# Kernel tuning notes

Measured on AMD Instinct MI355X. Metric: run time of the kernel, lower is better.

## Reference

```python
import jax, jax.numpy as jnp
import numpy as np

N_NODES = 100000
N_EDGES = 3200000
NODE_DIM = 32
EDGE_DIM = 16
LN_EPS = 1e-5


def setup_inputs() -> dict:
    key = jax.random.key(0)
    ks = jax.random.split(key, 12)
    zdim = 2 * NODE_DIM + EDGE_DIM  # 80
    s_lin = 1.0 / np.sqrt(zdim)
    s_out = 1.0 / np.sqrt(NODE_DIM)
    return {
        "x": jax.random.normal(ks[0], (N_NODES, NODE_DIM), jnp.float32),
        "edge_index": jax.random.randint(ks[1], (2, N_EDGES), 0, N_NODES, jnp.int32),
        "edge_attr": jax.random.normal(ks[2], (N_EDGES, EDGE_DIM), jnp.float32),
        "edge_weight": jax.random.uniform(ks[3], (N_EDGES,), jnp.float32),
        "lin_f_w": jax.random.uniform(ks[4], (zdim, NODE_DIM), jnp.float32, -s_lin, s_lin),
        "lin_f_b": jax.random.uniform(ks[5], (NODE_DIM,), jnp.float32, -s_lin, s_lin),
        "lin_s_w": jax.random.uniform(ks[6], (zdim, NODE_DIM), jnp.float32, -s_lin, s_lin),
        "lin_s_b": jax.random.uniform(ks[7], (NODE_DIM,), jnp.float32, -s_lin, s_lin),
        "ln_g": jnp.ones((NODE_DIM,), jnp.float32),
        "ln_b": jnp.zeros((NODE_DIM,), jnp.float32),
        "lin_w": jax.random.uniform(ks[8], (NODE_DIM, NODE_DIM), jnp.float32, -s_out, s_out),
        "lin_b": jax.random.uniform(ks[9], (NODE_DIM,), jnp.float32, -s_out, s_out),
    }


def reference(x, edge_index, edge_attr, edge_weight,
              lin_f_w, lin_f_b, lin_s_w, lin_s_b,
              ln_g, ln_b, lin_w, lin_b):
    src, dst = edge_index[0], edge_index[1]  # PyG: x_j = x[src], x_i = x[dst]
    # Gather + concat -> z [E, 2*node_dim + edge_dim]
    z = jnp.concatenate([x[dst], x[src], edge_attr], axis=-1)
    # Dual-linear gate: sigmoid(lin_f(z)) * softplus(lin_s(z)), scaled by edge_weight
    gate = jax.nn.sigmoid(z @ lin_f_w + lin_f_b)
    val = jax.nn.softplus(z @ lin_s_w + lin_s_b)
    msg = edge_weight[:, None] * gate * val  # [E, node_dim]
    # Scatter-add to target nodes
    agg = jax.ops.segment_sum(msg, dst, num_segments=x.shape[0])
    h = agg + x  # conv residual
    # LayerNorm
    mu = jnp.mean(h, axis=-1, keepdims=True)
    var = jnp.var(h, axis=-1, keepdims=True)
    h = (h - mu) * jax.lax.rsqrt(var + LN_EPS) * ln_g + ln_b
    # Linear + residual + ELU
    h = h @ lin_w + lin_b + x
    out = jax.nn.elu(h)
    return (out, edge_index, edge_attr, edge_weight)
```

## Files before the change

### kernel.cpp

```cpp
#include <hip/hip_runtime.h>
#include <hip/hip_fp16.h>
#include <math.h>

#define NODE_DIM 32
#define EDGE_DIM 16
#define WPC 64
#define MAXBLK 2500

typedef __attribute__((ext_vector_type(8))) short bf16x8;
typedef __attribute__((ext_vector_type(4))) short short4v;
typedef __attribute__((ext_vector_type(4))) float f32x4;

__device__ __forceinline__ short f2bf(float f) {
    union { float f; unsigned u; } v; v.f = f;
    unsigned r = v.u + 0x7FFFu + ((v.u >> 16) & 1u);
    return (short)(r >> 16);
}

__device__ __forceinline__ float fast_sigmoid(float v) {
    return __builtin_amdgcn_rcpf(1.0f + __expf(-v));
}
__device__ __forceinline__ float fast_softplus(float v) {
    float t = __expf(-fabsf(v));
    return fmaxf(v, 0.0f) + __logf(1.0f + t);
}

__global__ __launch_bounds__(256) void xconv_kernel(
    const float* __restrict__ x, short* __restrict__ xb, int ngroups)
{
    const int i = blockIdx.x * 256 + threadIdx.x;
    if (i >= ngroups) return;
    const float4* p = (const float4*)x + 2 * (size_t)i;
    float4 u0 = p[0], u1 = p[1];
    bf16x8 o;
    o[0]=f2bf(u0.x); o[1]=f2bf(u0.y); o[2]=f2bf(u0.z); o[3]=f2bf(u0.w);
    o[4]=f2bf(u1.x); o[5]=f2bf(u1.y); o[6]=f2bf(u1.z); o[7]=f2bf(u1.w);
    ((bf16x8*)xb)[i] = o;
}

__global__ __launch_bounds__(256, 4) void edge_kernel(
    const short* __restrict__ xb,
    const int*   __restrict__ ei,
    const float* __restrict__ ea,
    const float* __restrict__ ew,
    const float* __restrict__ Wf,
    const float* __restrict__ bfb,
    const float* __restrict__ Ws,
    const float* __restrict__ bsb,
    __half2* __restrict__ agg2,
    float* __restrict__ out_ei,
    float* __restrict__ out_ea,
    float* __restrict__ out_ew,
    int E)
{
    __shared__ short sea[4][WPC * EDGE_DIM];

    const int tid  = threadIdx.x;
    const int lane = tid & 63;
    const int wave = tid >> 6;
    const int kg   = lane >> 4;
    const int c16  = lane & 15;

    bf16x8 Bf[3][4];
    float biasv[4];
    #pragma unroll
    for (int ct = 0; ct < 4; ++ct) {
        const float* Wsrc = (ct < 2) ? Wf  : Ws;
        const float* bsrc = (ct < 2) ? bfb : bsb;
        const int ccc = 2 * c16 + (ct & 1);
        biasv[ct] = bsrc[ccc];
        #pragma unroll
        for (int m = 0; m < 3; ++m) {
            bf16x8 frag;
            #pragma unroll
            for (int j = 0; j < 8; ++j) {
                const int k = 32 * m + 8 * kg + j;
                const float wv = (k < 80) ? Wsrc[k * NODE_DIM + ccc] : 0.0f;
                frag[j] = f2bf(wv);
            }
            Bf[m][ct] = frag;
        }
    }

    const int wid    = blockIdx.x * 4 + wave;
    const int nwaves = gridDim.x * 4;

    for (int base = wid * WPC; base < E; base += nwaves * WPC) {
        const int e0 = base + lane;
        int srcv = 0, dstv = -1; float wv = 0.0f;
        if (e0 < E) {
            srcv = ei[e0];
            dstv = ei[E + e0];
            wv   = ew[e0];
            out_ei[e0]     = (float)srcv;
            out_ei[E + e0] = (float)dstv;
            out_ew[e0]     = wv;
        }
        {
            const float4* s4 = (const float4*)ea;
            float4*       d4 = (float4*)out_ea;
            const int fmax = E * 4;
            const int fb   = base * 4;
            #pragma unroll
            for (int t = 0; t < 4; ++t) {
                const int idx = fb + t * 64 + lane;
                if (idx < fmax) {
                    float4 v = s4[idx];
                    d4[idx] = v;
                    short4v sv = { f2bf(v.x), f2bf(v.y), f2bf(v.z), f2bf(v.w) };
                    *(short4v*)&sea[wave][(t * 64 + lane) * 4] = sv;
                }
            }
        }

        #pragma unroll 2
        for (int g = 0; g < 4; ++g) {
            const int sA   = g * 16 + c16;
            const int dstn = max(__shfl(dstv, sA), 0);
            const int srcn = max(__shfl(srcv, sA), 0);

            bf16x8 a0 = *(const bf16x8*)(xb + (size_t)dstn * NODE_DIM + 8 * kg);
            bf16x8 a1 = *(const bf16x8*)(xb + (size_t)srcn * NODE_DIM + 8 * kg);
            bf16x8 a2 = {0,0,0,0,0,0,0,0};
            if (kg < 2) {
                a2 = *(const bf16x8*)&sea[wave][sA * EDGE_DIM + 8 * kg];
            }

            f32x4 acc0 = {biasv[0], biasv[0], biasv[0], biasv[0]};
            f32x4 acc1 = {biasv[1], biasv[1], biasv[1], biasv[1]};
            f32x4 acc2 = {biasv[2], biasv[2], biasv[2], biasv[2]};
            f32x4 acc3 = {biasv[3], biasv[3], biasv[3], biasv[3]};

            acc0 = __builtin_amdgcn_mfma_f32_16x16x32_bf16(a0, Bf[0][0], acc0, 0, 0, 0);
            acc1 = __builtin_amdgcn_mfma_f32_16x16x32_bf16(a0, Bf[0][1], acc1, 0, 0, 0);
            acc2 = __builtin_amdgcn_mfma_f32_16x16x32_bf16(a0, Bf[0][2], acc2, 0, 0, 0);
            acc3 = __builtin_amdgcn_mfma_f32_16x16x32_bf16(a0, Bf[0][3], acc3, 0, 0, 0);
            acc0 = __builtin_amdgcn_mfma_f32_16x16x32_bf16(a1, Bf[1][0], acc0, 0, 0, 0);
            acc1 = __builtin_amdgcn_mfma_f32_16x16x32_bf16(a1, Bf[1][1], acc1, 0, 0, 0);
            acc2 = __builtin_amdgcn_mfma_f32_16x16x32_bf16(a1, Bf[1][2], acc2, 0, 0, 0);
            acc3 = __builtin_amdgcn_mfma_f32_16x16x32_bf16(a1, Bf[1][3], acc3, 0, 0, 0);
            acc0 = __builtin_amdgcn_mfma_f32_16x16x32_bf16(a2, Bf[2][0], acc0, 0, 0, 0);
            acc1 = __builtin_amdgcn_mfma_f32_16x16x32_bf16(a2, Bf[2][1], acc1, 0, 0, 0);
            acc2 = __builtin_amdgcn_mfma_f32_16x16x32_bf16(a2, Bf[2][2], acc2, 0, 0, 0);
            acc3 = __builtin_amdgcn_mfma_f32_16x16x32_bf16(a2, Bf[2][3], acc3, 0, 0, 0);

            const int rb = g * 16 + (kg << 2);
            #pragma unroll
            for (int r = 0; r < 4; ++r) {
                const int slot = rb + r;
                const int d    = __shfl(dstv, slot);
                const float w  = __shfl(wv,   slot);
                const float me = w * fast_sigmoid(acc0[r]) * fast_softplus(acc2[r]);
                const float mo = w * fast_sigmoid(acc1[r]) * fast_softplus(acc3[r]);
                if (d >= 0) {
                    __half2 hv = __floats2half2_rn(me, mo);
                    unsafeAtomicAdd(&agg2[(size_t)d * 16 + c16], hv);
                }
            }
        }
    }
}

__global__ __launch_bounds__(256) void node_kernel(
    const float* __restrict__ x,
    const __half2* __restrict__ agg2,
    const float* __restrict__ ln_g,
    const float* __restrict__ ln_b,
    const float* __restrict__ W,
    const float* __restrict__ b,
    float* __restrict__ out,
    int N)
{
    const int n = blockIdx.x * blockDim.x + threadIdx.x;
    if (n >= N) return;

    float xr[NODE_DIM], h[NODE_DIM];
    const float4*  xp = (const float4*)(x + (size_t)n * NODE_DIM);
    const __half2* ah = agg2 + (size_t)n * 16;

    float s = 0.0f, ss = 0.0f;
    #pragma unroll
    for (int i = 0; i < 8; ++i) {
        float4 xv = xp[i];
        float2 f0 = __half22float2(ah[2 * i]);
        float2 f1 = __half22float2(ah[2 * i + 1]);
        float hv0 = xv.x + f0.x, hv1 = xv.y + f0.y, hv2 = xv.z + f1.x, hv3 = xv.w + f1.y;
        xr[4*i+0] = xv.x; xr[4*i+1] = xv.y; xr[4*i+2] = xv.z; xr[4*i+3] = xv.w;
        h[4*i+0] = hv0; h[4*i+1] = hv1; h[4*i+2] = hv2; h[4*i+3] = hv3;
        s  += hv0 + hv1 + hv2 + hv3;
        ss += hv0*hv0 + hv1*hv1 + hv2*hv2 + hv3*hv3;
    }

    const float mu  = s * (1.0f / NODE_DIM);
    float var = ss * (1.0f / NODE_DIM) - mu * mu;
    var = fmaxf(var, 0.0f);
    const float rstd = __builtin_amdgcn_rsqf(var + 1e-5f);

    float acc[NODE_DIM];
    #pragma unroll
    for (int j = 0; j < NODE_DIM; ++j) acc[j] = b[j] + xr[j];

    #pragma unroll
    for (int k = 0; k < NODE_DIM; ++k) {
        float hn = (h[k] - mu) * rstd * ln_g[k] + ln_b[k];
        #pragma unroll
        for (int j = 0; j < NODE_DIM; ++j) {
            acc[j] = fmaf(hn, W[k * NODE_DIM + j], acc[j]);
        }
    }

    float4* op = (float4*)(out + (size_t)n * NODE_DIM);
    #pragma unroll
    for (int i = 0; i < 8; ++i) {
        float4 o;
        float a0 = acc[4*i+0], a1 = acc[4*i+1], a2 = acc[4*i+2], a3 = acc[4*i+3];
        o.x = (a0 > 0.0f) ? a0 : (__expf(a0) - 1.0f);
        o.y = (a1 > 0.0f) ? a1 : (__expf(a1) - 1.0f);
        o.z = (a2 > 0.0f) ? a2 : (__expf(a2) - 1.0f);
        o.w = (a3 > 0.0f) ? a3 : (__expf(a3) - 1.0f);
        op[i] = o;
    }
}

extern "C" void kernel_launch(void* const* d_in, const int* in_sizes, int n_in,
                              void* d_out, int out_size, void* d_ws, size_t ws_size,
                              hipStream_t stream)
{
    const float* x   = (const float*)d_in[0];
    const int*   ei  = (const int*)  d_in[1];
    const float* ea  = (const float*)d_in[2];
    const float* ew  = (const float*)d_in[3];
    const float* Wf  = (const float*)d_in[4];
    const float* bf  = (const float*)d_in[5];
    const float* Ws  = (const float*)d_in[6];
    const float* bs  = (const float*)d_in[7];
    const float* lg  = (const float*)d_in[8];
    const float* lb  = (const float*)d_in[9];
    const float* W   = (const float*)d_in[10];
    const float* b   = (const float*)d_in[11];

    const int E = in_sizes[3];
    const int N = in_sizes[0] / NODE_DIM;

    float* out    = (float*)d_out;
    float* out_x  = out;
    float* out_ei = out + (size_t)N * NODE_DIM;
    float* out_ea = out + (size_t)N * NODE_DIM + 2 * (size_t)E;
    float* out_ew = out_ea + (size_t)E * EDGE_DIM;

    __half2* agg2 = (__half2*)d_ws;
    short*   xbuf = (short*)((char*)d_ws + (size_t)N * 16 * sizeof(__half2));

    hipMemsetAsync(agg2, 0, (size_t)N * 16 * sizeof(__half2), stream);

    const int ngroups = N * NODE_DIM / 8;
    xconv_kernel<<<dim3((ngroups + 255) / 256), dim3(256), 0, stream>>>(x, xbuf, ngroups);

    int nblk = (E + 4 * WPC - 1) / (4 * WPC);
    if (nblk > MAXBLK) nblk = MAXBLK;
    edge_kernel<<<dim3(nblk), dim3(256), 0, stream>>>(
        xbuf, ei, ea, ew, Wf, bf, Ws, bs, agg2, out_ei, out_ea, out_ew, E);

    dim3 nb(256), ng((N + 255) / 256);
    node_kernel<<<ng, nb, 0, stream>>>(x, agg2, lg, lb, W, b, out_x, N);
}
```

Before: 281.9 us.

## Sort edges by destination via counting sort and combine same-node atomics

Adds histogram, two-level scan and scatter kernels that build a permutation grouping edges by destination node. The edge kernel then processes edges in that order and accumulates runs of consecutive edges with the same destination in registers before issuing one half2 atomic, cutting atomic traffic. In exchange it adds several extra kernel launches, a contended atomic histogram and scatter over all edges, a single-thread block-sum scan, and non-coalesced permuted reads of edge_attr and edge_weight.

Result: slower. 865.4 us (+207.0%).

```diff
diff --git a/kernel.cpp b/kernel.cpp
--- a/kernel.cpp
+++ b/kernel.cpp
@@ -6,6 +6,7 @@
 #define EDGE_DIM 16
 #define WPC 64
 #define MAXBLK 2500
+#define SCAN_BS 1024
 
 typedef __attribute__((ext_vector_type(8))) short bf16x8;
 typedef __attribute__((ext_vector_type(4))) short short4v;
@@ -36,6 +37,65 @@
     o[0]=f2bf(u0.x); o[1]=f2bf(u0.y); o[2]=f2bf(u0.z); o[3]=f2bf(u0.w);
     o[4]=f2bf(u1.x); o[5]=f2bf(u1.y); o[6]=f2bf(u1.z); o[7]=f2bf(u1.w);
     ((bf16x8*)xb)[i] = o;
+}
+
+__global__ __launch_bounds__(256) void hist_kernel(
+    const int* __restrict__ ei, int* __restrict__ cnt, int E)
+{
+    const int t = blockIdx.x * 256 + threadIdx.x;
+    if (t < E) atomicAdd(&cnt[ei[E + t]], 1);
+}
+
+__global__ __launch_bounds__(SCAN_BS) void bsum_kernel(
+    const int* __restrict__ cnt, int* __restrict__ bsum, int N)
+{
+    __shared__ int red[SCAN_BS];
+    const int t = blockIdx.x * SCAN_BS + threadIdx.x;
+    red[threadIdx.x] = (t < N) ? cnt[t] : 0;
+    __syncthreads();
+    for (int s = SCAN_BS / 2; s > 0; s >>= 1) {
+        if (threadIdx.x < s) red[threadIdx.x] += red[threadIdx.x + s];
+        __syncthreads();
+    }
+    if (threadIdx.x == 0) bsum[blockIdx.x] = red[0];
+}
+
+__global__ void scanb_kernel(int* __restrict__ bsum, int nb)
+{
+    if (blockIdx.x == 0 && threadIdx.x == 0) {
+        int acc = 0;
+        for (int i = 0; i < nb; ++i) { int v = bsum[i]; bsum[i] = acc; acc += v; }
+    }
+}
+
+__global__ __launch_bounds__(SCAN_BS) void woff_kernel(
+    const int* __restrict__ cnt, const int* __restrict__ bsum,
+    int* __restrict__ woff, int N)
+{
+    __shared__ int sc[SCAN_BS];
+    const int t = blockIdx.x * SCAN_BS + threadIdx.x;
+    const int v = (t < N) ? cnt[t] : 0;
+    sc[threadIdx.x] = v;
+    __syncthreads();
+    for (int s = 1; s < SCAN_BS; s <<= 1) {
+        int add = (threadIdx.x >= s) ? sc[threadIdx.x - s] : 0;
+        __syncthreads();
+        sc[threadIdx.x] += add;
+        __syncthreads();
+    }
+    if (t < N) woff[t] = bsum[blockIdx.x] + sc[threadIdx.x] - v;
+}
+
+__global__ __launch_bounds__(256) void scatter_kernel(
+    const int* __restrict__ ei, int* __restrict__ woff,
+    int* __restrict__ perm, int E)
+{
+    const int t = blockIdx.x * 256 + threadIdx.x;
+    if (t < E) {
+        const int d = ei[E + t];
+        const int pos = atomicAdd(&woff[d], 1);
+        perm[pos] = t;
+    }
 }
 
 __global__ __launch_bounds__(256, 4) void edge_kernel(
@@ -47,6 +107,7 @@
     const float* __restrict__ bfb,
     const float* __restrict__ Ws,
     const float* __restrict__ bsb,
+    const int*   __restrict__ perm,
     __half2* __restrict__ agg2,
     float* __restrict__ out_ei,
     float* __restrict__ out_ea,
@@ -86,34 +147,33 @@
     const int nwaves = gridDim.x * 4;
 
     for (int base = wid * WPC; base < E; base += nwaves * WPC) {
-        const int e0 = base + lane;
+        const int oe = base + lane;
+
+        if (oe < E) {
+            out_ei[oe]     = (float)ei[oe];
+            out_ei[E + oe] = (float)ei[E + oe];
+            out_ew[oe]     = ew[oe];
+        }
+
         int srcv = 0, dstv = -1; float wv = 0.0f;
-        if (e0 < E) {
-            srcv = ei[e0];
-            dstv = ei[E + e0];
-            wv   = ew[e0];
-            out_ei[e0]     = (float)srcv;
-            out_ei[E + e0] = (float)dstv;
-            out_ew[e0]     = wv;
-        }
-        {
-            const float4* s4 = (const float4*)ea;
-            float4*       d4 = (float4*)out_ea;
-            const int fmax = E * 4;
-            const int fb   = base * 4;
+        if (oe < E) {
+            const int p = perm[oe];
+            srcv = ei[p]; dstv = ei[E + p]; wv = ew[p];
+            const float4* s4 = (const float4*)(ea + (size_t)p * EDGE_DIM);
+            float4*       d4 = (float4*)(out_ea + (size_t)p * EDGE_DIM);
             #pragma unroll
             for (int t = 0; t < 4; ++t) {
-                const int idx = fb + t * 64 + lane;
-                if (idx < fmax) {
-                    float4 v = s4[idx];
-                    d4[idx] = v;
-                    short4v sv = { f2bf(v.x), f2bf(v.y), f2bf(v.z), f2bf(v.w) };
-                    *(short4v*)&sea[wave][(t * 64 + lane) * 4] = sv;
-                }
+                float4 v = s4[t];
+                d4[t] = v;
+                short4v sv = { f2bf(v.x), f2bf(v.y), f2bf(v.z), f2bf(v.w) };
+                *(short4v*)&sea[wave][lane * EDGE_DIM + t * 4] = sv;
             }
         }
 
-        #pragma unroll 2
+        float accE = 0.0f, accO = 0.0f;
+        int dprev = -1;
+
+        #pragma unroll
         for (int g = 0; g < 4; ++g) {
             const int sA   = g * 16 + c16;
             const int dstn = max(__shfl(dstv, sA), 0);
@@ -152,12 +212,18 @@
                 const float w  = __shfl(wv,   slot);
                 const float me = w * fast_sigmoid(acc0[r]) * fast_softplus(acc2[r]);
                 const float mo = w * fast_sigmoid(acc1[r]) * fast_softplus(acc3[r]);
-                if (d >= 0) {
-                    __half2 hv = __floats2half2_rn(me, mo);
-                    unsafeAtomicAdd(&agg2[(size_t)d * 16 + c16], hv);
+                if (d != dprev) {
+                    if (dprev >= 0)
+                        unsafeAtomicAdd(&agg2[(size_t)dprev * 16 + c16],
+                                        __floats2half2_rn(accE, accO));
+                    accE = 0.0f; accO = 0.0f; dprev = d;
                 }
+                accE += me; accO += mo;
             }
         }
+        if (dprev >= 0)
+            unsafeAtomicAdd(&agg2[(size_t)dprev * 16 + c16],
+                            __floats2half2_rn(accE, accO));
     }
 }
 
@@ -248,18 +314,31 @@
     float* out_ea = out + (size_t)N * NODE_DIM + 2 * (size_t)E;
     float* out_ew = out_ea + (size_t)E * EDGE_DIM;
 
-    __half2* agg2 = (__half2*)d_ws;
-    short*   xbuf = (short*)((char*)d_ws + (size_t)N * 16 * sizeof(__half2));
+    char* wsp = (char*)d_ws;
+    __half2* agg2 = (__half2*)wsp;                 wsp += (size_t)N * 16 * sizeof(__half2);
+    short*   xbuf = (short*)wsp;                   wsp += (size_t)N * NODE_DIM * sizeof(short);
+    int*     cnt  = (int*)wsp;                     wsp += (size_t)N * sizeof(int);
+    int*     woff = (int*)wsp;                     wsp += (size_t)N * sizeof(int);
+    int*     bsum = (int*)wsp;                     wsp += 4096;
+    int*     perm = (int*)wsp;
 
     hipMemsetAsync(agg2, 0, (size_t)N * 16 * sizeof(__half2), stream);
+    hipMemsetAsync(cnt,  0, (size_t)N * sizeof(int), stream);
 
     const int ngroups = N * NODE_DIM / 8;
     xconv_kernel<<<dim3((ngroups + 255) / 256), dim3(256), 0, stream>>>(x, xbuf, ngroups);
+
+    const int nb1 = (N + SCAN_BS - 1) / SCAN_BS;
+    hist_kernel<<<dim3((E + 255) / 256), dim3(256), 0, stream>>>(ei, cnt, E);
+    bsum_kernel<<<dim3(nb1), dim3(SCAN_BS), 0, stream>>>(cnt, bsum, N);
+    scanb_kernel<<<dim3(1), dim3(64), 0, stream>>>(bsum, nb1);
+    woff_kernel<<<dim3(nb1), dim3(SCAN_BS), 0, stream>>>(cnt, bsum, woff, N);
+    scatter_kernel<<<dim3((E + 255) / 256), dim3(256), 0, stream>>>(ei, woff, perm, E);
 
     int nblk = (E + 4 * WPC - 1) / (4 * WPC);
     if (nblk > MAXBLK) nblk = MAXBLK;
     edge_kernel<<<dim3(nblk), dim3(256), 0, stream>>>(
-        xbuf, ei, ea, ew, Wf, bf, Ws, bs, agg2, out_ei, out_ea, out_ew, E);
+        xbuf, ei, ea, ew, Wf, bf, Ws, bs, perm, agg2, out_ei, out_ea, out_ew, E);
 
     dim3 nb(256), ng((N + 255) / 256);
     node_kernel<<<ng, nb, 0, stream>>>(x, agg2, lg, lb, W, b, out_x, N);
```
